# Performance work log

Hardware: AMD Instinct MI355X
Metric: run time of the kernel (lower is better)

The kernel has to match this reference:

```python
import jax, jax.numpy as jnp
import numpy as np

D_MODEL = 1024
N_HEAD = 16


def setup_inputs() -> dict:
    key = jax.random.key(0)
    k1, k2, k3 = jax.random.split(key, 3)
    scale = 1.0 / np.sqrt(D_MODEL)
    x = jax.random.normal(k1, (1, 4096, D_MODEL), dtype=jnp.float32)
    # nn.Linear weights stored as [out, in]; applied as x @ W.T
    w_attn = jax.random.normal(k2, (3 * D_MODEL, D_MODEL), dtype=jnp.float32) * scale
    w_proj = jax.random.normal(k3, (D_MODEL, D_MODEL), dtype=jnp.float32) * scale
    return {"x": x, "w_attn": w_attn, "w_proj": w_proj}


def reference(x, w_attn, w_proj):
    B, T, C = x.shape
    H = N_HEAD
    hd = C // H
    qkv = x @ w_attn.T                      # [B, T, 3C]
    q, k, v = jnp.split(qkv, 3, axis=-1)
    # [B, T, C] -> [B, H, T, hd]
    q = q.reshape(B, T, H, hd).transpose(0, 2, 1, 3)
    k = k.reshape(B, T, H, hd).transpose(0, 2, 1, 3)
    v = v.reshape(B, T, H, hd).transpose(0, 2, 1, 3)
    att = jnp.einsum("bhqd,bhkd->bhqk", q, k) * (1.0 / np.sqrt(hd))  # [B,H,T,T]
    causal = jnp.tril(jnp.ones((T, T), dtype=bool))
    att = jnp.where(causal[None, None], att, -jnp.inf)
    att = jax.nn.softmax(att, axis=-1)
    y = jnp.einsum("bhqk,bhkd->bhqd", att, v)  # [B,H,T,hd]
    y = y.transpose(0, 2, 1, 3).reshape(B, T, C)
    return y @ w_proj.T
```

## Files before the change

kernel.cpp:

```cpp
#include <hip/hip_runtime.h>
#include <hip/hip_bf16.h>
#include <stdint.h>

typedef __bf16 bf16x8 __attribute__((ext_vector_type(8)));
typedef float f32x4 __attribute__((ext_vector_type(4)));

#define T_SEQ 4096
#define C_DIM 1024
#define H_NUM 16
#define HD 64
#define C3 3072
#define NEG_BIG (-30000.0f)

__device__ __forceinline__ unsigned short f2bf(float f) {
    uint32_t u = __builtin_bit_cast(uint32_t, f);
    u += 0x7fffu + ((u >> 16) & 1u);
    return (unsigned short)(u >> 16);
}

__device__ __forceinline__ uint32_t pk_bf16(float a, float b) {
    __hip_bfloat162 h = __float22bfloat162_rn(float2{a, b});
    uint32_t u;
    __builtin_memcpy(&u, &h, sizeof(u));
    return u;
}

__device__ __forceinline__ bf16x8 ld_bf8(const unsigned short* p) {
    return *reinterpret_cast<const bf16x8*>(p);
}

__device__ __forceinline__ void async_g2l16(const unsigned short* g, unsigned short* l) {
    __builtin_amdgcn_global_load_lds(
        (const __attribute__((address_space(1))) void*)g,
        (__attribute__((address_space(3))) void*)l, 16, 0, 0);
}

__device__ __forceinline__ void store_c(unsigned short* C, size_t idx, float v) { C[idx] = f2bf(v); }
__device__ __forceinline__ void store_c(float* C, size_t idx, float v)          { C[idx] = v; }

__device__ __forceinline__ void cvt8(const float* src, unsigned short* dst) {
    float4 f0 = *(const float4*)src;
    float4 f1 = *(const float4*)(src + 4);
    union { uint32_t w[4]; uint4 q; } t;
    t.w[0] = pk_bf16(f0.x, f0.y);
    t.w[1] = pk_bf16(f0.z, f0.w);
    t.w[2] = pk_bf16(f1.x, f1.y);
    t.w[3] = pk_bf16(f1.z, f1.w);
    *(uint4*)dst = t.q;
}

__global__ void cvt_xw(const float* __restrict__ x, const float* __restrict__ wa,
                       unsigned short* __restrict__ xb, unsigned short* __restrict__ wab) {
    int i = (blockIdx.x * blockDim.x + threadIdx.x) * 8;
    if (i < T_SEQ * C_DIM) cvt8(x + i, xb + i);
    else {
        int k = i - T_SEQ * C_DIM;
        if (k < C3 * C_DIM) cvt8(wa + k, wab + k);
    }
}

__global__ void cvt_f32_bf16(const float* __restrict__ src, unsigned short* __restrict__ dst, int n) {
    int i = (blockIdx.x * blockDim.x + threadIdx.x) * 8;
    if (i >= n) return;
    cvt8(src + i, dst + i);
}

__global__ __launch_bounds__(256) void v_transpose(
    const unsigned short* __restrict__ qkv, unsigned short* __restrict__ Vt)
{
    __shared__ unsigned short tile[64][72];
    const int t0 = blockIdx.x * 64, c0 = blockIdx.y * 64;
    const int r = threadIdx.x >> 2, q = threadIdx.x & 3;

    const unsigned short* src = qkv + (size_t)(t0 + r) * C3 + 2 * C_DIM + c0 + q * 16;
    *(uint4*)&tile[r][q * 16]     = *(const uint4*)src;
    *(uint4*)&tile[r][q * 16 + 8] = *(const uint4*)(src + 8);
    __syncthreads();

    union { unsigned short u[16]; uint4 v[2]; } o;
    #pragma unroll
    for (int j = 0; j < 16; ++j) o.u[j] = tile[q * 16 + j][r];
    unsigned short* dst = Vt + (size_t)(c0 + r) * T_SEQ + t0 + q * 16;
    *(uint4*)dst       = o.v[0];
    *(uint4*)(dst + 8) = o.v[1];
}

template <typename TC>
__global__ __launch_bounds__(256, 2) void gemm_bt(
    const unsigned short* __restrict__ A, const unsigned short* __restrict__ B,
    TC* __restrict__ C, int M, int N, int K)
{
    __shared__ __attribute__((aligned(16))) unsigned short As[128 * 32];
    __shared__ __attribute__((aligned(16))) unsigned short Bs[128 * 32];

    const int tid  = threadIdx.x;
    const int wave = tid >> 6, lane = tid & 63;
    const int quad = lane >> 4, l16 = lane & 15;
    const int wm = wave >> 1, wn = wave & 1;
    const int m0 = blockIdx.y * 128, n0 = blockIdx.x * 128;

    const int srow = wave * 32 + (lane >> 2);
    const int scol = (lane & 3) * 8;

    f32x4 acc[4][4] = {};

    for (int k0 = 0; k0 < K; k0 += 32) {
        {
            const unsigned short* ga = A + (size_t)(m0 + srow) * K + k0 + scol;
            const unsigned short* gb = B + (size_t)(n0 + srow) * K + k0 + scol;
            unsigned short* la = As + (wave * 32) * 32;
            unsigned short* lb = Bs + (wave * 32) * 32;
            async_g2l16(ga, la);
            async_g2l16(ga + (size_t)16 * K, la + 16 * 32);
            async_g2l16(gb, lb);
            async_g2l16(gb + (size_t)16 * K, lb + 16 * 32);
        }
        __syncthreads();

        bf16x8 af[4], bf[4];
        #pragma unroll
        for (int i = 0; i < 4; ++i) {
            af[i] = ld_bf8(As + (wm * 64 + i * 16 + l16) * 32 + quad * 8);
            bf[i] = ld_bf8(Bs + (wn * 64 + i * 16 + l16) * 32 + quad * 8);
        }
        #pragma unroll
        for (int mt = 0; mt < 4; ++mt)
            #pragma unroll
            for (int nt = 0; nt < 4; ++nt)
                acc[mt][nt] = __builtin_amdgcn_mfma_f32_16x16x32_bf16(
                    af[mt], bf[nt], acc[mt][nt], 0, 0, 0);
        __syncthreads();
    }

    #pragma unroll
    for (int mt = 0; mt < 4; ++mt)
        #pragma unroll
        for (int nt = 0; nt < 4; ++nt)
            #pragma unroll
            for (int r = 0; r < 4; ++r) {
                int row = m0 + wm * 64 + mt * 16 + quad * 4 + r;
                int col = n0 + wn * 64 + nt * 16 + l16;
                store_c(C, (size_t)row * N + col, acc[mt][nt][r]);
            }
}

#define PL_STRIDE 2848

template <bool MASK>
__device__ __forceinline__ void fa6_tile(
    const unsigned short* Ksb, const unsigned short* Vsb, unsigned short* pbuf,
    const bf16x8 qf[2][2], f32x4 o[2][4], float* l_part,
    int k0, int q_abs0, int quad, int l16, int sw, int fo0, int fo1)
{
    const unsigned short* krow = Ksb + l16 * 64;
    bf16x8 kf[4][2];
    #pragma unroll
    for (int s = 0; s < 4; ++s) {
        kf[s][0] = ld_bf8(krow + s * 1024 + fo0);
        kf[s][1] = ld_bf8(krow + s * 1024 + fo1);
    }

    #pragma unroll
    for (int qs = 0; qs < 2; ++qs) {
        f32x4 st[4];
        #pragma unroll
        for (int s = 0; s < 4; ++s) {
            f32x4 z = {};
            z = __builtin_amdgcn_mfma_f32_16x16x32_bf16(kf[s][0], qf[qs][0], z, 0, 0, 0);
            st[s] = __builtin_amdgcn_mfma_f32_16x16x32_bf16(kf[s][1], qf[qs][1], z, 0, 0, 0);
        }
        float ts = 0.f;
        #pragma unroll
        for (int s = 0; s < 4; ++s)
            #pragma unroll
            for (int r = 0; r < 4; ++r) {
                float v = st[s][r];
                if (MASK) {
                    int key = k0 + s * 16 + quad * 4 + r;
                    v = (key <= q_abs0 + qs * 16) ? v : NEG_BIG;
                }
                float e = __builtin_amdgcn_exp2f(v);
                st[s][r] = e;
                ts += e;
            }
        l_part[qs] += ts;

        unsigned short* prow = pbuf + (qs * 16 + l16) * 64;
        #pragma unroll
        for (int s = 0; s < 4; ++s) {
            int g = 2 * s + (quad >> 1);
            uint2 pk;
            pk.x = pk_bf16(st[s][0], st[s][1]);
            pk.y = pk_bf16(st[s][2], st[s][3]);
            *(uint2*)((char*)prow + (g ^ sw) * 16 + 8 * (quad & 1)) = pk;
        }
    }

    const unsigned short* vrow = Vsb + l16 * 64;
    bf16x8 vf[4][2];
    #pragma unroll
    for (int c = 0; c < 4; ++c) {
        vf[c][0] = ld_bf8(vrow + c * 1024 + fo0);
        vf[c][1] = ld_bf8(vrow + c * 1024 + fo1);
    }
    #pragma unroll
    for (int qs = 0; qs < 2; ++qs) {
        const unsigned short* prow = pbuf + (qs * 16 + l16) * 64;
        bf16x8 pf0 = ld_bf8(prow + fo0);
        bf16x8 pf1 = ld_bf8(prow + fo1);
        #pragma unroll
        for (int c = 0; c < 4; ++c) {
            o[qs][c] = __builtin_amdgcn_mfma_f32_16x16x32_bf16(vf[c][0], pf0, o[qs][c], 0, 0, 0);
            o[qs][c] = __builtin_amdgcn_mfma_f32_16x16x32_bf16(vf[c][1], pf1, o[qs][c], 0, 0, 0);
        }
    }
}

__global__ __launch_bounds__(256, 2) void flash_attn6(
    const unsigned short* __restrict__ qkv,
    const unsigned short* __restrict__ Vt,
    unsigned short* __restrict__ Y)
{
    __shared__ __attribute__((aligned(16))) unsigned short Ks[2][64 * 64];
    __shared__ __attribute__((aligned(16))) unsigned short Vs[2][64 * 64];
    __shared__ __attribute__((aligned(16))) unsigned short Pl[4][PL_STRIDE];

    const int tid  = threadIdx.x;
    const int wave = tid >> 6, lane = tid & 63;
    const int quad = lane >> 4, l16 = lane & 15;

    const int bi = blockIdx.x;
    const int rr = bi >> 8, ss = bi & 255;
    const int h  = ss & 15;
    const int j  = ss >> 4;
    const int qb = rr ? (31 - j) : j;

    const int q0w    = qb * 128 + wave * 32;
    const int q_abs0 = q0w + l16;
    const int sw  = l16 & 7;
    const int fo0 = (quad ^ sw) * 8;
    const int fo1 = ((quad + 4) ^ sw) * 8;

    bf16x8 qf[2][2];
    {
        const float QS = 0.125f * 1.44269504f;
        #pragma unroll
        for (int qs = 0; qs < 2; ++qs) {
            const unsigned short* qp =
                qkv + (size_t)(q0w + qs * 16 + l16) * C3 + h * HD + quad * 8;
            bf16x8 a = ld_bf8(qp), b = ld_bf8(qp + 32);
            #pragma unroll
            for (int i = 0; i < 8; ++i) {
                qf[qs][0][i] = (__bf16)((float)a[i] * QS);
                qf[qs][1][i] = (__bf16)((float)b[i] * QS);
            }
        }
    }

    const int srow = lane >> 3;
    const int schunk = (lane & 7) ^ srow;
    const unsigned short* kp0 =
        qkv + (size_t)(wave * 16 + srow) * C3 + C_DIM + h * HD + schunk * 8;
    const unsigned short* kp1 = kp0 + (size_t)8 * C3;
    const unsigned short* vp0 =
        Vt + (size_t)(h * HD + wave * 16 + srow) * T_SEQ + schunk * 8;
    const unsigned short* vp1 = vp0 + (size_t)8 * T_SEQ;
    unsigned short* lk0  = Ks[0] + (wave * 16) * 64;
    unsigned short* lk0b = lk0 + 8 * 64;
    unsigned short* lv0  = Vs[0] + (wave * 16) * 64;
    unsigned short* lv0b = lv0 + 8 * 64;
    const int lds_db = 64 * 64;

    f32x4 o[2][4] = {};
    float l_part[2] = {0.f, 0.f};
    unsigned short* pbuf = Pl[wave];

    const int ntiles = 2 * qb + 2;
    const int mask_t = 2 * qb + (wave >> 1);

    async_g2l16(kp0, lk0);  async_g2l16(kp1, lk0b);
    async_g2l16(vp0, lv0);  async_g2l16(vp1, lv0b);
    kp0 += (size_t)64 * C3; kp1 += (size_t)64 * C3;
    vp0 += 64;              vp1 += 64;

    for (int t = 0; t < ntiles; ++t) {
        __syncthreads();
        const int b = t & 1;
        if (t + 1 < ntiles) {
            const int nb = 1 - b;
            async_g2l16(kp0, lk0 + nb * lds_db);
            async_g2l16(kp1, lk0b + nb * lds_db);
            async_g2l16(vp0, lv0 + nb * lds_db);
            async_g2l16(vp1, lv0b + nb * lds_db);
            kp0 += (size_t)64 * C3; kp1 += (size_t)64 * C3;
            vp0 += 64;              vp1 += 64;
        }
        if (t < mask_t) {
            fa6_tile<false>(Ks[b], Vs[b], pbuf, qf, o, l_part,
                            t * 64, q_abs0, quad, l16, sw, fo0, fo1);
        } else if (t == mask_t) {
            fa6_tile<true>(Ks[b], Vs[b], pbuf, qf, o, l_part,
                           t * 64, q_abs0, quad, l16, sw, fo0, fo1);
        }
    }

    #pragma unroll
    for (int qs = 0; qs < 2; ++qs) {
        float l = l_part[qs];
        l += __shfl_xor(l, 16, 64);
        l += __shfl_xor(l, 32, 64);
        float inv_l = 1.f / l;
        #pragma unroll
        for (int c = 0; c < 4; ++c) {
            union { uint32_t w[2]; uint2 q; } t;
            t.w[0] = pk_bf16(o[qs][c][0] * inv_l, o[qs][c][1] * inv_l);
            t.w[1] = pk_bf16(o[qs][c][2] * inv_l, o[qs][c][3] * inv_l);
            *(uint2*)(Y + (size_t)(q_abs0 + qs * 16) * C_DIM + h * HD + c * 16 + quad * 4) = t.q;
        }
    }
}

extern "C" void kernel_launch(void* const* d_in, const int* in_sizes, int n_in,
                              void* d_out, int out_size, void* d_ws, size_t ws_size,
                              hipStream_t stream) {
    const float* x      = (const float*)d_in[0];
    const float* w_attn = (const float*)d_in[1];
    const float* w_proj = (const float*)d_in[2];
    float* out = (float*)d_out;

    unsigned short* qkv = (unsigned short*)d_ws;
    unsigned short* xb  = qkv + (size_t)T_SEQ * C3;
    unsigned short* y   = xb;
    unsigned short* wpb = qkv;
    unsigned short* Vt  = (unsigned short*)d_out;
    unsigned short* wab = Vt + (size_t)C_DIM * T_SEQ;

    cvt_xw<<<(T_SEQ * C_DIM + C3 * C_DIM) / 8 / 256, 256, 0, stream>>>(x, w_attn, xb, wab);

    gemm_bt<unsigned short>
        <<<dim3(C3 / 128, T_SEQ / 128), 256, 0, stream>>>(xb, wab, qkv, T_SEQ, C3, C_DIM);

    v_transpose<<<dim3(T_SEQ / 64, C_DIM / 64), 256, 0, stream>>>(qkv, Vt);

    flash_attn6<<<dim3(512), 256, 0, stream>>>(qkv, Vt, y);

    cvt_f32_bf16<<<(C_DIM * C_DIM / 8 + 255) / 256, 256, 0, stream>>>(w_proj, wpb, C_DIM * C_DIM);
    gemm_bt<float>
        <<<dim3(C_DIM / 128, T_SEQ / 128), 256, 0, stream>>>(y, wpb, out, T_SEQ, C_DIM, C_DIM);
}
```

Baseline: 220.5 us.

## Split flash attention into 64-query blocks of two waves with more blocks

The flash attention kernel now uses 128-thread blocks covering 64 query rows instead of 256-thread blocks covering 128, launching 1024 blocks. Block-to-query mapping is reordered in four groups to balance causal work, and the P scratch buffer shrinks to an unpadded 32x64 tile per wave. This removes the idle waves in the diagonal tile and improves load balance across CUs. In exchange each block reloads K/V per 64 queries, doubling global K/V traffic, and the unpadded P buffer may cause LDS bank conflicts.

```diff
diff --git a/kernel.cpp b/kernel.cpp
--- a/kernel.cpp
+++ b/kernel.cpp
@@ -144,10 +144,8 @@
             }
 }
 
-#define PL_STRIDE 2848
-
 template <bool MASK>
-__device__ __forceinline__ void fa6_tile(
+__device__ __forceinline__ void fa7_tile(
     const unsigned short* Ksb, const unsigned short* Vsb, unsigned short* pbuf,
     const bf16x8 qf[2][2], f32x4 o[2][4], float* l_part,
     int k0, int q_abs0, int quad, int l16, int sw, int fo0, int fo1)
@@ -216,14 +214,14 @@
     }
 }
 
-__global__ __launch_bounds__(256, 2) void flash_attn6(
+__global__ __launch_bounds__(128, 2) void flash_attn7(
     const unsigned short* __restrict__ qkv,
     const unsigned short* __restrict__ Vt,
     unsigned short* __restrict__ Y)
 {
     __shared__ __attribute__((aligned(16))) unsigned short Ks[2][64 * 64];
     __shared__ __attribute__((aligned(16))) unsigned short Vs[2][64 * 64];
-    __shared__ __attribute__((aligned(16))) unsigned short Pl[4][PL_STRIDE];
+    __shared__ __attribute__((aligned(16))) unsigned short Pl[2][32 * 64];
 
     const int tid  = threadIdx.x;
     const int wave = tid >> 6, lane = tid & 63;
@@ -233,9 +231,9 @@
     const int rr = bi >> 8, ss = bi & 255;
     const int h  = ss & 15;
     const int j  = ss >> 4;
-    const int qb = rr ? (31 - j) : j;
-
-    const int q0w    = qb * 128 + wave * 32;
+    const int qb = (rr == 0) ? j : (rr == 1) ? 63 - j : (rr == 2) ? 16 + j : 47 - j;
+
+    const int q0w    = qb * 64 + wave * 32;
     const int q_abs0 = q0w + l16;
     const int sw  = l16 & 7;
     const int fo0 = (quad ^ sw) * 8;
@@ -259,47 +257,42 @@
 
     const int srow = lane >> 3;
     const int schunk = (lane & 7) ^ srow;
-    const unsigned short* kp0 =
-        qkv + (size_t)(wave * 16 + srow) * C3 + C_DIM + h * HD + schunk * 8;
-    const unsigned short* kp1 = kp0 + (size_t)8 * C3;
-    const unsigned short* vp0 =
-        Vt + (size_t)(h * HD + wave * 16 + srow) * T_SEQ + schunk * 8;
-    const unsigned short* vp1 = vp0 + (size_t)8 * T_SEQ;
-    unsigned short* lk0  = Ks[0] + (wave * 16) * 64;
-    unsigned short* lk0b = lk0 + 8 * 64;
-    unsigned short* lv0  = Vs[0] + (wave * 16) * 64;
-    unsigned short* lv0b = lv0 + 8 * 64;
+    const unsigned short* kp =
+        qkv + (size_t)(wave * 32 + srow) * C3 + C_DIM + h * HD + schunk * 8;
+    const unsigned short* vp =
+        Vt + (size_t)(h * HD + wave * 32 + srow) * T_SEQ + schunk * 8;
+    unsigned short* lk = Ks[0] + (wave * 32) * 64;
+    unsigned short* lv = Vs[0] + (wave * 32) * 64;
     const int lds_db = 64 * 64;
+    const size_t kstep = (size_t)8 * C3;
+    const size_t vstep = (size_t)8 * T_SEQ;
+
+    auto stage = [&](int b) {
+        #pragma unroll
+        for (int jj = 0; jj < 4; ++jj) {
+            async_g2l16(kp + jj * kstep, lk + b * lds_db + jj * 8 * 64);
+            async_g2l16(vp + jj * vstep, lv + b * lds_db + jj * 8 * 64);
+        }
+    };
 
     f32x4 o[2][4] = {};
     float l_part[2] = {0.f, 0.f};
     unsigned short* pbuf = Pl[wave];
 
-    const int ntiles = 2 * qb + 2;
-    const int mask_t = 2 * qb + (wave >> 1);
-
-    async_g2l16(kp0, lk0);  async_g2l16(kp1, lk0b);
-    async_g2l16(vp0, lv0);  async_g2l16(vp1, lv0b);
-    kp0 += (size_t)64 * C3; kp1 += (size_t)64 * C3;
-    vp0 += 64;              vp1 += 64;
+    const int ntiles = qb + 1;
+    stage(0);
+    kp += (size_t)64 * C3; vp += 64;
 
     for (int t = 0; t < ntiles; ++t) {
         __syncthreads();
         const int b = t & 1;
         if (t + 1 < ntiles) {
-            const int nb = 1 - b;
-            async_g2l16(kp0, lk0 + nb * lds_db);
-            async_g2l16(kp1, lk0b + nb * lds_db);
-            async_g2l16(vp0, lv0 + nb * lds_db);
-            async_g2l16(vp1, lv0b + nb * lds_db);
-            kp0 += (size_t)64 * C3; kp1 += (size_t)64 * C3;
-            vp0 += 64;              vp1 += 64;
-        }
-        if (t < mask_t) {
-            fa6_tile<false>(Ks[b], Vs[b], pbuf, qf, o, l_part,
+            stage(1 - b);
+            kp += (size_t)64 * C3; vp += 64;
+            fa7_tile<false>(Ks[b], Vs[b], pbuf, qf, o, l_part,
                             t * 64, q_abs0, quad, l16, sw, fo0, fo1);
-        } else if (t == mask_t) {
-            fa6_tile<true>(Ks[b], Vs[b], pbuf, qf, o, l_part,
+        } else {
+            fa7_tile<true>(Ks[b], Vs[b], pbuf, qf, o, l_part,
                            t * 64, q_abs0, quad, l16, sw, fo0, fo1);
         }
     }
@@ -342,7 +335,7 @@
 
     v_transpose<<<dim3(T_SEQ / 64, C_DIM / 64), 256, 0, stream>>>(qkv, Vt);
 
-    flash_attn6<<<dim3(512), 256, 0, stream>>>(qkv, Vt, y);
+    flash_attn7<<<dim3(1024), 128, 0, stream>>>(qkv, Vt, y);
 
     cvt_f32_bf16<<<(C_DIM * C_DIM / 8 + 255) / 256, 256, 0, stream>>>(w_proj, wpb, C_DIM * C_DIM);
     gemm_bt<float>
```

Result: no change. 218.7 us (-0.8%).
